# Optimization experiments

Hardware: AMD Instinct MI355X
Metric: run time of the kernel (lower is better)

## Reference

```python
import jax, jax.numpy as jnp
import numpy as np

B, T, C = 128, 256, 384
H, D = 6, 64

def setup_inputs() -> dict:
    key = jax.random.key(0)
    ks = jax.random.split(key, 6)
    s = 1.0 / np.sqrt(C)
    return {
        "x": jax.random.normal(ks[0], (B, T, C), dtype=jnp.float32),
        "Wq": jax.random.normal(ks[1], (H, C, D), dtype=jnp.float32) * s,
        "Wk": jax.random.normal(ks[2], (H, C, D), dtype=jnp.float32) * s,
        "Wv": jax.random.normal(ks[3], (H, C, D), dtype=jnp.float32) * s,
        "Wp": jax.random.normal(ks[4], (C, C), dtype=jnp.float32) * s,
        "bp": jnp.zeros((C,), dtype=jnp.float32),
    }

def reference(x, Wq, Wk, Wv, Wp, bp):
    # per-head projections (all heads at once): [B,T,C] x [H,C,D] -> [B,H,T,D]
    q = jnp.einsum("btc,hcd->bhtd", x, Wq)
    k = jnp.einsum("btc,hcd->bhtd", x, Wk)
    v = jnp.einsum("btc,hcd->bhtd", x, Wv)
    scale = 1.0 / jnp.sqrt(jnp.asarray(D, dtype=x.dtype))
    # scores [B,H,T,T], causal mask, softmax
    wei = jnp.einsum("bhqd,bhkd->bhqk", q, k) * scale
    causal = jnp.tril(jnp.ones((T, T), dtype=bool))
    wei = jnp.where(causal, wei, -jnp.inf)
    wei = jax.nn.softmax(wei, axis=-1)
    # dropout layers are identity in eval mode
    out = jnp.einsum("bhqk,bhkd->bhqd", wei, v)
    # concat heads: [B,T,H*D]
    out = out.transpose(0, 2, 1, 3).reshape(B, T, H * D)
    return out @ Wp + bp
```

## Files before the change

kernel.cpp:

```cpp
#include <hip/hip_runtime.h>
#include <stdint.h>


typedef __attribute__((ext_vector_type(8))) short bf16x8;
typedef __attribute__((ext_vector_type(4))) float f32x4;
typedef __attribute__((ext_vector_type(16))) float f32x16;

__device__ __forceinline__ unsigned short f2b(float f) {
    union { float f; unsigned int u; } v; v.f = f;
    unsigned int u = v.u + 0x7fffu + ((v.u >> 16) & 1u);
    return (unsigned short)(u >> 16);
}

__device__ __forceinline__ unsigned int pk2(float lo, float hi) {
    return (unsigned int)f2b(lo) | ((unsigned int)f2b(hi) << 16);
}

__device__ __forceinline__ void gload_lds16(const void* g, void* lds) {
    auto gp = reinterpret_cast<const __attribute__((address_space(1))) uint32_t*>(
        reinterpret_cast<uintptr_t>(g));
    auto lp = reinterpret_cast<__attribute__((address_space(3))) uint32_t*>(
        reinterpret_cast<uintptr_t>(lds));
    __builtin_amdgcn_global_load_lds(gp, lp, 16, 0, 0);
}

#define SBAR0() __builtin_amdgcn_sched_barrier(0)


__global__ void cvt_x_kernel(const float* __restrict__ x, unsigned short* __restrict__ xb, int n8) {
    int i = blockIdx.x * 256 + threadIdx.x;
    if (i >= n8) return;
    float4 a = ((const float4*)x)[(size_t)i * 2];
    float4 b = ((const float4*)x)[(size_t)i * 2 + 1];
    uint4 o;
    o.x = pk2(a.x, a.y); o.y = pk2(a.z, a.w);
    o.z = pk2(b.x, b.y); o.w = pk2(b.z, b.w);
    ((uint4*)xb)[i] = o;
}

__global__ void cvt_w_kernel(const float* __restrict__ Wq, const float* __restrict__ Wk,
                             const float* __restrict__ Wv, const float* __restrict__ Wp,
                             unsigned short* __restrict__ wt, unsigned short* __restrict__ wpt) {
    int i = blockIdx.x * 256 + threadIdx.x;
    if (i >= 589824) return;
    if (i < 442368) {
        int j = i / 384, c = i - j * 384;
        int p = j / 384, rem = j - p * 384;
        int h = rem >> 6, d = rem & 63;
        const float* W = (p == 0) ? Wq : ((p == 1) ? Wk : Wv);
        wt[i] = f2b(W[(size_t)(h * 384 + c) * 64 + d]);
    } else {
        int i2 = i - 442368;
        int n = i2 / 384, c = i2 - n * 384;
        wpt[i2] = f2b(Wp[(size_t)c * 384 + n]);
    }
}


__global__ __launch_bounds__(256, 3) void gemm_qkv(
    const unsigned short* __restrict__ xb,
    const unsigned short* __restrict__ wt,
    unsigned short* __restrict__ qO,
    unsigned short* __restrict__ kO,
    unsigned short* __restrict__ vO)
{
    extern __shared__ __align__(16) unsigned short smem[];
    unsigned short* AsBase = smem;
    unsigned short* BsBase = smem + 12288;

    const int tid  = threadIdx.x;
    const int lane = tid & 63;
    const int w    = tid >> 6;
    const int wm = w >> 1, wn = w & 1;

    const int flat = blockIdx.y * 9 + blockIdx.x;
    const int swz = (flat & 7) * 288 + (flat >> 3);
    const int bx = swz % 9, by = swz / 9;
    const int col0 = bx * 128;
    const int row0 = by * 128;

    const unsigned short* Abase = xb + (size_t)row0 * 384;
    const unsigned short* Bbase = wt + (size_t)col0 * 384;

    f32x4 acc[4][4];
#pragma unroll
    for (int mf = 0; mf < 4; ++mf)
#pragma unroll
        for (int nf = 0; nf < 4; ++nf)
#pragma unroll
            for (int r = 0; r < 4; ++r) acc[mf][nf][r] = 0.f;

    const int ci0 = tid;
    const int ci1 = tid + 256;
    const unsigned short* aSrc0 = Abase + (size_t)(ci0 >> 2) * 384 + (ci0 & 3) * 8;
    const unsigned short* aSrc1 = Abase + (size_t)(ci1 >> 2) * 384 + (ci1 & 3) * 8;
    const unsigned short* bSrc0 = Bbase + (size_t)(ci0 >> 2) * 384 + (ci0 & 3) * 8;
    const unsigned short* bSrc1 = Bbase + (size_t)(ci1 >> 2) * 384 + (ci1 & 3) * 8;
    const int cb = w * 64;

    auto STAGE = [&](int buf, int kt) {
        const int k0_ = kt * 32;
        gload_lds16(aSrc0 + k0_, AsBase + buf * 4096 + (cb + 0) * 8);
        gload_lds16(bSrc0 + k0_, BsBase + buf * 4096 + (cb + 0) * 8);
        gload_lds16(aSrc1 + k0_, AsBase + buf * 4096 + (cb + 256) * 8);
        gload_lds16(bSrc1 + k0_, BsBase + buf * 4096 + (cb + 256) * 8);
    };

    auto COMPUTE = [&](int buf) {
        const unsigned short* A = AsBase + buf * 4096;
        const unsigned short* B = BsBase + buf * 4096;
        bf16x8 aF[4], bF[4];
#pragma unroll
        for (int mf = 0; mf < 4; ++mf)
            aF[mf] = *(const bf16x8*)&A[(wm * 64 + mf * 16 + (lane & 15)) * 32 + (lane >> 4) * 8];
#pragma unroll
        for (int nf = 0; nf < 4; ++nf)
            bF[nf] = *(const bf16x8*)&B[(wn * 64 + nf * 16 + (lane & 15)) * 32 + (lane >> 4) * 8];
#pragma unroll
        for (int mf = 0; mf < 4; ++mf)
#pragma unroll
            for (int nf = 0; nf < 4; ++nf)
                acc[mf][nf] = __builtin_amdgcn_mfma_f32_16x16x32_bf16(aF[mf], bF[nf], acc[mf][nf], 0, 0, 0);
    };

    STAGE(0, 0);
    STAGE(1, 1);
    SBAR0();
    int bufS = 2, bufC = 0;
    for (int t = 0; t < 10; ++t) {
        STAGE(bufS, t + 2);
        bufS = (bufS == 2) ? 0 : bufS + 1;
        SBAR0();
        asm volatile("s_waitcnt vmcnt(8)" ::: "memory");
        SBAR0();
        __builtin_amdgcn_s_barrier();
        SBAR0();
        COMPUTE(bufC);
        bufC = (bufC == 2) ? 0 : bufC + 1;
        SBAR0();
        __builtin_amdgcn_s_barrier();
        SBAR0();
    }
    asm volatile("s_waitcnt vmcnt(4)" ::: "memory");
    SBAR0();
    __builtin_amdgcn_s_barrier();
    SBAR0();
    COMPUTE(1);
    SBAR0();
    __builtin_amdgcn_s_barrier();
    SBAR0();
    asm volatile("s_waitcnt vmcnt(0)" ::: "memory");
    SBAR0();
    __builtin_amdgcn_s_barrier();
    SBAR0();
    COMPUTE(2);
    __syncthreads();

    unsigned short* Ct = smem;
    const int co = tid & 15;
    const int rr = tid >> 4;
    const int colg = col0 + co * 8;
    const int p = colg / 384;
    const int rem = colg - p * 384;
    const int h = rem >> 6;
    const int d = rem & 63;
    unsigned short* dst = (p == 0) ? qO : ((p == 1) ? kO : vO);

#pragma unroll
    for (int ph = 0; ph < 2; ++ph) {
        if (wm == ph) {
#pragma unroll
            for (int mf = 0; mf < 4; ++mf)
#pragma unroll
                for (int nf = 0; nf < 4; ++nf)
#pragma unroll
                    for (int r = 0; r < 4; ++r)
                        Ct[(mf * 16 + (lane >> 4) * 4 + r) * 136 + wn * 64 + nf * 16 + (lane & 15)] =
                            f2b(acc[mf][nf][r]);
        }
        __syncthreads();
#pragma unroll
        for (int it = 0; it < 4; ++it) {
            const int r_loc = it * 16 + rr;
            const int m = row0 + ph * 64 + r_loc;
            const int b = m >> 8, t = m & 255;
            uint4 val = *(const uint4*)&Ct[r_loc * 136 + co * 8];
            *(uint4*)&dst[(size_t)((b * 6 + h) * 256 + t) * 64 + d] = val;
        }
        __syncthreads();
    }
}


__global__ __launch_bounds__(512) void attn_kernel(
    const unsigned short* __restrict__ Qg,
    const unsigned short* __restrict__ Kg,
    const unsigned short* __restrict__ Vg,
    unsigned short* __restrict__ Og)
{
    __shared__ __align__(16) unsigned short Ks[256 * 72];
    __shared__ __align__(16) unsigned short Vs[64 * 264];
    __shared__ __align__(16) unsigned short Ot[8 * 32 * 72];
    const int bh = blockIdx.x;
    const int b = bh / 6, h = bh - b * 6;
    const int tid = threadIdx.x;
    const int lane = tid & 63;
    const int w = tid >> 6;
    const int lo = lane & 31, hi = lane >> 5;

    const unsigned short* kg = Kg + (size_t)bh * 256 * 64;
#pragma unroll
    for (int j = 0; j < 4; ++j) {
        int chunk = tid + 512 * j;
        int key = chunk >> 3, dc = (chunk & 7) * 8;
        *(uint4*)&Ks[key * 72 + dc] = *(const uint4*)&kg[key * 64 + dc];
    }
    {
        const unsigned short* vg = Vg + (size_t)bh * 256 * 64;
        uint32_t* Vs32 = (uint32_t*)Vs;
#pragma unroll
        for (int i = 0; i < 2; ++i) {
            int u = tid + 512 * i;
            int t2 = (u & 31) | ((u >> 8) << 5);
            int dm = (u >> 5) & 7;
            uint4 r0 = *(const uint4*)&vg[(2 * t2 + 0) * 64 + dm * 8];
            uint4 r1 = *(const uint4*)&vg[(2 * t2 + 1) * 64 + dm * 8];
            const unsigned short* e0 = (const unsigned short*)&r0;
            const unsigned short* e1 = (const unsigned short*)&r1;
#pragma unroll
            for (int j = 0; j < 8; ++j)
                Vs32[(dm * 8 + j) * 132 + t2] = (uint32_t)e0[j] | ((uint32_t)e1[j] << 16);
        }
    }
    __syncthreads();

    const int q0 = w * 32;
    const unsigned short* qg = Qg + (size_t)bh * 256 * 64 + (size_t)(q0 + lo) * 64 + hi * 8;
    bf16x8 qF[4];
#pragma unroll
    for (int dc = 0; dc < 4; ++dc) qF[dc] = *(const bf16x8*)(qg + dc * 16);

    float m = -1e30f, ssum = 0.f;
    f32x16 o0, o1;
#pragma unroll
    for (int r = 0; r < 16; ++r) { o0[r] = 0.f; o1[r] = 0.f; }

    for (int kt = 0; kt <= w; ++kt) {
        f32x16 s;
#pragma unroll
        for (int r = 0; r < 16; ++r) s[r] = 0.f;
#pragma unroll
        for (int dc = 0; dc < 4; ++dc) {
            bf16x8 aK = *(const bf16x8*)&Ks[(kt * 32 + lo) * 72 + dc * 16 + hi * 8];
            s = __builtin_amdgcn_mfma_f32_32x32x16_bf16(aK, qF[dc], s, 0, 0, 0);
        }
        float p[16];
        float pmax = -1e30f;
        const bool diag = (kt == w);
#pragma unroll
        for (int r = 0; r < 16; ++r) {
            float sv = s[r] * 0.125f;
            const int keyl = (r & 3) + 8 * (r >> 2) + 4 * hi;
            if (diag && keyl > lo) sv = -1e30f;
            p[r] = sv;
            pmax = fmaxf(pmax, sv);
        }
        pmax = fmaxf(pmax, __shfl_xor(pmax, 32, 64));
        const float mn = fmaxf(m, pmax);
        const float sf = __expf(m - mn);
        m = mn;
        ssum *= sf;
#pragma unroll
        for (int r = 0; r < 16; ++r) { o0[r] *= sf; o1[r] *= sf; }
        float rs = 0.f;
#pragma unroll
        for (int r = 0; r < 16; ++r) { p[r] = __expf(p[r] - m); rs += p[r]; }
        rs += __shfl_xor(rs, 32, 64);
        ssum += rs;

        union { unsigned short u[16]; bf16x8 v[2]; } P;
        {
            float recv[4];
#pragma unroll
            for (int j2 = 0; j2 < 4; ++j2) {
                float sendv = hi ? p[j2] : p[4 + j2];
                recv[j2] = __shfl_xor(sendv, 32, 64);
            }
#pragma unroll
            for (int i = 0; i < 4; ++i) P.u[i]     = f2b(hi ? recv[i] : p[i]);
#pragma unroll
            for (int i = 0; i < 4; ++i) P.u[4 + i] = f2b(hi ? p[4 + i] : recv[i]);
        }
        {
            float recv[4];
#pragma unroll
            for (int j2 = 0; j2 < 4; ++j2) {
                float sendv = hi ? p[8 + j2] : p[12 + j2];
                recv[j2] = __shfl_xor(sendv, 32, 64);
            }
#pragma unroll
            for (int i = 0; i < 4; ++i) P.u[8 + i]  = f2b(hi ? recv[i] : p[8 + i]);
#pragma unroll
            for (int i = 0; i < 4; ++i) P.u[12 + i] = f2b(hi ? p[12 + i] : recv[i]);
        }

#pragma unroll
        for (int kc = 0; kc < 2; ++kc) {
            bf16x8 aV0 = *(const bf16x8*)&Vs[lo * 264 + kt * 32 + kc * 16 + hi * 8];
            o0 = __builtin_amdgcn_mfma_f32_32x32x16_bf16(aV0, P.v[kc], o0, 0, 0, 0);
            bf16x8 aV1 = *(const bf16x8*)&Vs[(32 + lo) * 264 + kt * 32 + kc * 16 + hi * 8];
            o1 = __builtin_amdgcn_mfma_f32_32x32x16_bf16(aV1, P.v[kc], o1, 0, 0, 0);
        }
    }

    const float inv = 1.f / ssum;
    {
        uint32_t* ot32 = (uint32_t*)&Ot[w * 32 * 72];
#pragma unroll
        for (int g = 0; g < 4; ++g) {
            const int dbase0 = 8 * g + 4 * hi;
            uint32_t w0 = pk2(o0[4 * g + 0] * inv, o0[4 * g + 1] * inv);
            uint32_t w1 = pk2(o0[4 * g + 2] * inv, o0[4 * g + 3] * inv);
            int dw = lo * 36 + (dbase0 >> 1);
            ot32[dw] = w0;
            ot32[dw + 1] = w1;
            uint32_t w2 = pk2(o1[4 * g + 0] * inv, o1[4 * g + 1] * inv);
            uint32_t w3 = pk2(o1[4 * g + 2] * inv, o1[4 * g + 3] * inv);
            int dw1 = lo * 36 + ((32 + dbase0) >> 1);
            ot32[dw1] = w2;
            ot32[dw1 + 1] = w3;
        }
    }
    __syncthreads();
    {
        const unsigned short* ot = &Ot[w * 32 * 72];
        const int q = lane >> 1;
        const int half = (lane & 1) * 32;
        unsigned short* og = Og + (size_t)(b * 256 + q0 + q) * 384 + h * 64 + half;
#pragma unroll
        for (int jj = 0; jj < 4; ++jj) {
            uint4 val = *(const uint4*)&ot[q * 72 + half + jj * 8];
            *(uint4*)&og[jj * 8] = val;
        }
    }
}


__global__ __launch_bounds__(256, 3) void gemm_proj(
    const unsigned short* __restrict__ ob,
    const unsigned short* __restrict__ wpt,
    const float* __restrict__ bp,
    float* __restrict__ out)
{
    __shared__ __align__(16) unsigned short As[3][128 * 32];
    __shared__ __align__(16) unsigned short Bs[3][128 * 32];
    const int tid  = threadIdx.x;
    const int lane = tid & 63;
    const int w    = tid >> 6;
    const int wm = w >> 1, wn = w & 1;

    const int flat = blockIdx.y * 3 + blockIdx.x;
    const int swz = (flat & 7) * 96 + (flat >> 3);
    const int bx = swz % 3, by = swz / 3;
    const int col0 = bx * 128;
    const int row0 = by * 128;

    const unsigned short* Abase = ob  + (size_t)row0 * 384;
    const unsigned short* Bbase = wpt + (size_t)col0 * 384;

    f32x4 acc[4][4];
#pragma unroll
    for (int mf = 0; mf < 4; ++mf)
#pragma unroll
        for (int nf = 0; nf < 4; ++nf)
#pragma unroll
            for (int r = 0; r < 4; ++r) acc[mf][nf][r] = 0.f;

    const int ci0 = tid;
    const int ci1 = tid + 256;
    const unsigned short* aSrc0 = Abase + (size_t)(ci0 >> 2) * 384 + (ci0 & 3) * 8;
    const unsigned short* aSrc1 = Abase + (size_t)(ci1 >> 2) * 384 + (ci1 & 3) * 8;
    const unsigned short* bSrc0 = Bbase + (size_t)(ci0 >> 2) * 384 + (ci0 & 3) * 8;
    const unsigned short* bSrc1 = Bbase + (size_t)(ci1 >> 2) * 384 + (ci1 & 3) * 8;
    const int cb = w * 64;

    auto STAGE = [&](int buf, int kt) {
        const int k0_ = kt * 32;
        gload_lds16(aSrc0 + k0_, (unsigned short*)As[buf] + (cb + 0) * 8);
        gload_lds16(bSrc0 + k0_, (unsigned short*)Bs[buf] + (cb + 0) * 8);
        gload_lds16(aSrc1 + k0_, (unsigned short*)As[buf] + (cb + 256) * 8);
        gload_lds16(bSrc1 + k0_, (unsigned short*)Bs[buf] + (cb + 256) * 8);
    };

    auto COMPUTE = [&](int buf) {
        const unsigned short* A = As[buf];
        const unsigned short* B = Bs[buf];
        bf16x8 aF[4], bF[4];
#pragma unroll
        for (int mf = 0; mf < 4; ++mf)
            aF[mf] = *(const bf16x8*)&A[(wm * 64 + mf * 16 + (lane & 15)) * 32 + (lane >> 4) * 8];
#pragma unroll
        for (int nf = 0; nf < 4; ++nf)
            bF[nf] = *(const bf16x8*)&B[(wn * 64 + nf * 16 + (lane & 15)) * 32 + (lane >> 4) * 8];
#pragma unroll
        for (int mf = 0; mf < 4; ++mf)
#pragma unroll
            for (int nf = 0; nf < 4; ++nf)
                acc[mf][nf] = __builtin_amdgcn_mfma_f32_16x16x32_bf16(aF[mf], bF[nf], acc[mf][nf], 0, 0, 0);
    };

    STAGE(0, 0);
    STAGE(1, 1);
    SBAR0();
    int bufS = 2, bufC = 0;
    for (int t = 0; t < 10; ++t) {
        STAGE(bufS, t + 2);
        bufS = (bufS == 2) ? 0 : bufS + 1;
        SBAR0();
        asm volatile("s_waitcnt vmcnt(8)" ::: "memory");
        SBAR0();
        __builtin_amdgcn_s_barrier();
        SBAR0();
        COMPUTE(bufC);
        bufC = (bufC == 2) ? 0 : bufC + 1;
        SBAR0();
        __builtin_amdgcn_s_barrier();
        SBAR0();
    }
    asm volatile("s_waitcnt vmcnt(4)" ::: "memory");
    SBAR0();
    __builtin_amdgcn_s_barrier();
    SBAR0();
    COMPUTE(1);
    SBAR0();
    __builtin_amdgcn_s_barrier();
    SBAR0();
    asm volatile("s_waitcnt vmcnt(0)" ::: "memory");
    SBAR0();
    __builtin_amdgcn_s_barrier();
    SBAR0();
    COMPUTE(2);

#pragma unroll
    for (int nf = 0; nf < 4; ++nf) {
        const int col = col0 + wn * 64 + nf * 16 + (lane & 15);
        const float bias = bp[col];
#pragma unroll
        for (int mf = 0; mf < 4; ++mf) {
            const int mbase = row0 + wm * 64 + mf * 16 + ((lane >> 4) * 4);
#pragma unroll
            for (int r = 0; r < 4; ++r) {
                const int mrow = mbase + r;
                out[(size_t)mrow * 384 + col] = acc[mf][nf][r] + bias;
            }
        }
    }
}


extern "C" void kernel_launch(void* const* d_in, const int* in_sizes, int n_in,
                              void* d_out, int out_size, void* d_ws, size_t ws_size,
                              hipStream_t stream) {
    const float* x  = (const float*)d_in[0];
    const float* Wq = (const float*)d_in[1];
    const float* Wk = (const float*)d_in[2];
    const float* Wv = (const float*)d_in[3];
    const float* Wp = (const float*)d_in[4];
    const float* bp = (const float*)d_in[5];
    float* out = (float*)d_out;

    char* ws = (char*)d_ws;
    unsigned short* xb  = (unsigned short*)(ws);
    unsigned short* qb  = (unsigned short*)(ws + 25165824);
    unsigned short* kb  = (unsigned short*)(ws + 50331648);
    unsigned short* vb  = (unsigned short*)(ws + 75497472);
    unsigned short* wt  = (unsigned short*)(ws + 100663296);
    unsigned short* wpt = (unsigned short*)(ws + 101548032);

    cvt_x_kernel<<<6144, 256, 0, stream>>>(x, xb, 1572864);
    cvt_w_kernel<<<2304, 256, 0, stream>>>(Wq, Wk, Wv, Wp, wt, wpt);
    gemm_qkv<<<dim3(9, 256), 256, 49152, stream>>>(xb, wt, qb, kb, vb);
    attn_kernel<<<768, 512, 0, stream>>>(qb, kb, vb, xb);
    gemm_proj<<<dim3(3, 256), 256, 0, stream>>>(xb, wpt, bp, out);
}
```

Baseline: 118.9 us.

## Fuse x fp32-to-bf16 conversion into QKV GEMM A-tile loading

Removes the separate x conversion kernel. gemm_qkv now loads fp32 x straight into registers, converts it to bf16 and writes it to double-buffered LDS, while B still arrives through async global-to-LDS loads. The pipeline drops from triple to double buffering, occupancy hint rises to 4, and the attention kernel's output staging now reuses the K/V LDS through dynamic shared memory. This saves one full write and reread of the bf16 x copy, at the cost of reading fp32 x (twice the bytes) once for each of the 9 column tiles, plus register-path conversion work inside the GEMM loop.

```diff
diff --git a/kernel.cpp b/kernel.cpp
--- a/kernel.cpp
+++ b/kernel.cpp
@@ -26,17 +26,6 @@
 
 #define SBAR0() __builtin_amdgcn_sched_barrier(0)
 
-
-__global__ void cvt_x_kernel(const float* __restrict__ x, unsigned short* __restrict__ xb, int n8) {
-    int i = blockIdx.x * 256 + threadIdx.x;
-    if (i >= n8) return;
-    float4 a = ((const float4*)x)[(size_t)i * 2];
-    float4 b = ((const float4*)x)[(size_t)i * 2 + 1];
-    uint4 o;
-    o.x = pk2(a.x, a.y); o.y = pk2(a.z, a.w);
-    o.z = pk2(b.x, b.y); o.w = pk2(b.z, b.w);
-    ((uint4*)xb)[i] = o;
-}
 
 __global__ void cvt_w_kernel(const float* __restrict__ Wq, const float* __restrict__ Wk,
                              const float* __restrict__ Wv, const float* __restrict__ Wp,
@@ -57,16 +46,18 @@
 }
 
 
-__global__ __launch_bounds__(256, 3) void gemm_qkv(
-    const unsigned short* __restrict__ xb,
+__global__ __launch_bounds__(256, 4) void gemm_qkv(
+    const float* __restrict__ x,
     const unsigned short* __restrict__ wt,
     unsigned short* __restrict__ qO,
     unsigned short* __restrict__ kO,
     unsigned short* __restrict__ vO)
 {
     extern __shared__ __align__(16) unsigned short smem[];
-    unsigned short* AsBase = smem;
-    unsigned short* BsBase = smem + 12288;
+    unsigned short* As0 = smem;
+    unsigned short* As1 = smem + 4096;
+    unsigned short* Bs0 = smem + 8192;
+    unsigned short* Bs1 = smem + 12288;
 
     const int tid  = threadIdx.x;
     const int lane = tid & 63;
@@ -79,8 +70,290 @@
     const int col0 = bx * 128;
     const int row0 = by * 128;
 
-    const unsigned short* Abase = xb + (size_t)row0 * 384;
-    const unsigned short* Bbase = wt + (size_t)col0 * 384;
+    f32x4 acc[4][4];
+#pragma unroll
+    for (int mf = 0; mf < 4; ++mf)
+#pragma unroll
+        for (int nf = 0; nf < 4; ++nf)
+#pragma unroll
+            for (int r = 0; r < 4; ++r) acc[mf][nf][r] = 0.f;
+
+    const int ci0 = tid;
+    const int ci1 = tid + 256;
+    const float* aS0 = x + (size_t)(row0 + (ci0 >> 2)) * 384 + (ci0 & 3) * 8;
+    const float* aS1 = x + (size_t)(row0 + (ci1 >> 2)) * 384 + (ci1 & 3) * 8;
+    const unsigned short* bS0 = wt + (size_t)(col0 + (ci0 >> 2)) * 384 + (ci0 & 3) * 8;
+    const unsigned short* bS1 = wt + (size_t)(col0 + (ci1 >> 2)) * 384 + (ci1 & 3) * 8;
+    const int cb = w * 64;
+
+    float4 aReg0, aReg1, aReg2, aReg3;
+    auto LOADA = [&](int kt) {
+        const float* p0 = aS0 + kt * 32;
+        const float* p1 = aS1 + kt * 32;
+        aReg0 = *(const float4*)(p0);
+        aReg1 = *(const float4*)(p0 + 4);
+        aReg2 = *(const float4*)(p1);
+        aReg3 = *(const float4*)(p1 + 4);
+    };
+    auto WRITEA = [&](unsigned short* As) {
+        uint4 w0 = make_uint4(pk2(aReg0.x, aReg0.y), pk2(aReg0.z, aReg0.w),
+                              pk2(aReg1.x, aReg1.y), pk2(aReg1.z, aReg1.w));
+        uint4 w1 = make_uint4(pk2(aReg2.x, aReg2.y), pk2(aReg2.z, aReg2.w),
+                              pk2(aReg3.x, aReg3.y), pk2(aReg3.z, aReg3.w));
+        *(uint4*)&As[ci0 * 8] = w0;
+        *(uint4*)&As[ci1 * 8] = w1;
+    };
+    auto STAGEB = [&](unsigned short* Bs, int kt) {
+        gload_lds16(bS0 + kt * 32, Bs + (cb + 0) * 8);
+        gload_lds16(bS1 + kt * 32, Bs + (cb + 256) * 8);
+    };
+    auto COMPUTE = [&](const unsigned short* A, const unsigned short* B) {
+        bf16x8 aF[4], bF[4];
+#pragma unroll
+        for (int mf = 0; mf < 4; ++mf)
+            aF[mf] = *(const bf16x8*)&A[(wm * 64 + mf * 16 + (lane & 15)) * 32 + (lane >> 4) * 8];
+#pragma unroll
+        for (int nf = 0; nf < 4; ++nf)
+            bF[nf] = *(const bf16x8*)&B[(wn * 64 + nf * 16 + (lane & 15)) * 32 + (lane >> 4) * 8];
+#pragma unroll
+        for (int mf = 0; mf < 4; ++mf)
+#pragma unroll
+            for (int nf = 0; nf < 4; ++nf)
+                acc[mf][nf] = __builtin_amdgcn_mfma_f32_16x16x32_bf16(aF[mf], bF[nf], acc[mf][nf], 0, 0, 0);
+    };
+
+    LOADA(0);
+    STAGEB(Bs0, 0);
+    WRITEA(As0);
+    __syncthreads();
+
+    for (int t = 0; t < 12; ++t) {
+        unsigned short* Acur = (t & 1) ? As1 : As0;
+        unsigned short* Bcur = (t & 1) ? Bs1 : Bs0;
+        unsigned short* Anx  = (t & 1) ? As0 : As1;
+        unsigned short* Bnx  = (t & 1) ? Bs0 : Bs1;
+        if (t < 11) {
+            LOADA(t + 1);
+            STAGEB(Bnx, t + 1);
+        }
+        COMPUTE(Acur, Bcur);
+        if (t < 11) WRITEA(Anx);
+        __syncthreads();
+    }
+
+    unsigned short* Ct = smem;
+    const int co = tid & 15;
+    const int rr = tid >> 4;
+    const int colg = col0 + co * 8;
+    const int p = colg / 384;
+    const int rem = colg - p * 384;
+    const int h = rem >> 6;
+    const int d = rem & 63;
+    unsigned short* dst = (p == 0) ? qO : ((p == 1) ? kO : vO);
+
+#pragma unroll
+    for (int ph = 0; ph < 2; ++ph) {
+        if (wm == ph) {
+#pragma unroll
+            for (int mf = 0; mf < 4; ++mf)
+#pragma unroll
+                for (int nf = 0; nf < 4; ++nf)
+#pragma unroll
+                    for (int r = 0; r < 4; ++r)
+                        Ct[(mf * 16 + (lane >> 4) * 4 + r) * 136 + wn * 64 + nf * 16 + (lane & 15)] =
+                            f2b(acc[mf][nf][r]);
+        }
+        __syncthreads();
+#pragma unroll
+        for (int it = 0; it < 4; ++it) {
+            const int r_loc = it * 16 + rr;
+            const int m = row0 + ph * 64 + r_loc;
+            const int b = m >> 8, t = m & 255;
+            uint4 val = *(const uint4*)&Ct[r_loc * 136 + co * 8];
+            *(uint4*)&dst[(size_t)((b * 6 + h) * 256 + t) * 64 + d] = val;
+        }
+        __syncthreads();
+    }
+}
+
+
+__global__ __launch_bounds__(512, 4) void attn_kernel(
+    const unsigned short* __restrict__ Qg,
+    const unsigned short* __restrict__ Kg,
+    const unsigned short* __restrict__ Vg,
+    unsigned short* __restrict__ Og)
+{
+    extern __shared__ __align__(16) unsigned short asmem[];
+    unsigned short* Ks = asmem;
+    unsigned short* Vs = asmem + 256 * 72;
+    unsigned short* Ot = asmem;
+    const int bh = blockIdx.x;
+    const int b = bh / 6, h = bh - b * 6;
+    const int tid = threadIdx.x;
+    const int lane = tid & 63;
+    const int w = tid >> 6;
+    const int lo = lane & 31, hi = lane >> 5;
+
+    const unsigned short* kg = Kg + (size_t)bh * 256 * 64;
+#pragma unroll
+    for (int j = 0; j < 4; ++j) {
+        int chunk = tid + 512 * j;
+        int key = chunk >> 3, dc = (chunk & 7) * 8;
+        *(uint4*)&Ks[key * 72 + dc] = *(const uint4*)&kg[key * 64 + dc];
+    }
+    {
+        const unsigned short* vg = Vg + (size_t)bh * 256 * 64;
+        uint32_t* Vs32 = (uint32_t*)Vs;
+#pragma unroll
+        for (int i = 0; i < 2; ++i) {
+            int u = tid + 512 * i;
+            int t2 = (u & 31) | ((u >> 8) << 5);
+            int dm = (u >> 5) & 7;
+            uint4 r0 = *(const uint4*)&vg[(2 * t2 + 0) * 64 + dm * 8];
+            uint4 r1 = *(const uint4*)&vg[(2 * t2 + 1) * 64 + dm * 8];
+            const unsigned short* e0 = (const unsigned short*)&r0;
+            const unsigned short* e1 = (const unsigned short*)&r1;
+#pragma unroll
+            for (int j = 0; j < 8; ++j)
+                Vs32[(dm * 8 + j) * 132 + t2] = (uint32_t)e0[j] | ((uint32_t)e1[j] << 16);
+        }
+    }
+    __syncthreads();
+
+    const int q0 = w * 32;
+    const unsigned short* qg = Qg + (size_t)bh * 256 * 64 + (size_t)(q0 + lo) * 64 + hi * 8;
+    bf16x8 qF[4];
+#pragma unroll
+    for (int dc = 0; dc < 4; ++dc) qF[dc] = *(const bf16x8*)(qg + dc * 16);
+
+    float m = -1e30f, ssum = 0.f;
+    f32x16 o0, o1;
+#pragma unroll
+    for (int r = 0; r < 16; ++r) { o0[r] = 0.f; o1[r] = 0.f; }
+
+    for (int kt = 0; kt <= w; ++kt) {
+        f32x16 s;
+#pragma unroll
+        for (int r = 0; r < 16; ++r) s[r] = 0.f;
+#pragma unroll
+        for (int dc = 0; dc < 4; ++dc) {
+            bf16x8 aK = *(const bf16x8*)&Ks[(kt * 32 + lo) * 72 + dc * 16 + hi * 8];
+            s = __builtin_amdgcn_mfma_f32_32x32x16_bf16(aK, qF[dc], s, 0, 0, 0);
+        }
+        float p[16];
+        float pmax = -1e30f;
+        const bool diag = (kt == w);
+#pragma unroll
+        for (int r = 0; r < 16; ++r) {
+            float sv = s[r] * 0.125f;
+            const int keyl = (r & 3) + 8 * (r >> 2) + 4 * hi;
+            if (diag && keyl > lo) sv = -1e30f;
+            p[r] = sv;
+            pmax = fmaxf(pmax, sv);
+        }
+        pmax = fmaxf(pmax, __shfl_xor(pmax, 32, 64));
+        const float mn = fmaxf(m, pmax);
+        const float sf = __expf(m - mn);
+        m = mn;
+        ssum *= sf;
+#pragma unroll
+        for (int r = 0; r < 16; ++r) { o0[r] *= sf; o1[r] *= sf; }
+        float rs = 0.f;
+#pragma unroll
+        for (int r = 0; r < 16; ++r) { p[r] = __expf(p[r] - m); rs += p[r]; }
+        rs += __shfl_xor(rs, 32, 64);
+        ssum += rs;
+
+        union { unsigned short u[16]; bf16x8 v[2]; } P;
+        {
+            float recv[4];
+#pragma unroll
+            for (int j2 = 0; j2 < 4; ++j2) {
+                float sendv = hi ? p[j2] : p[4 + j2];
+                recv[j2] = __shfl_xor(sendv, 32, 64);
+            }
+#pragma unroll
+            for (int i = 0; i < 4; ++i) P.u[i]     = f2b(hi ? recv[i] : p[i]);
+#pragma unroll
+            for (int i = 0; i < 4; ++i) P.u[4 + i] = f2b(hi ? p[4 + i] : recv[i]);
+        }
+        {
+            float recv[4];
+#pragma unroll
+            for (int j2 = 0; j2 < 4; ++j2) {
+                float sendv = hi ? p[8 + j2] : p[12 + j2];
+                recv[j2] = __shfl_xor(sendv, 32, 64);
+            }
+#pragma unroll
+            for (int i = 0; i < 4; ++i) P.u[8 + i]  = f2b(hi ? recv[i] : p[8 + i]);
+#pragma unroll
+            for (int i = 0; i < 4; ++i) P.u[12 + i] = f2b(hi ? p[12 + i] : recv[i]);
+        }
+
+#pragma unroll
+        for (int kc = 0; kc < 2; ++kc) {
+            bf16x8 aV0 = *(const bf16x8*)&Vs[lo * 264 + kt * 32 + kc * 16 + hi * 8];
+            o0 = __builtin_amdgcn_mfma_f32_32x32x16_bf16(aV0, P.v[kc], o0, 0, 0, 0);
+            bf16x8 aV1 = *(const bf16x8*)&Vs[(32 + lo) * 264 + kt * 32 + kc * 16 + hi * 8];
+            o1 = __builtin_amdgcn_mfma_f32_32x32x16_bf16(aV1, P.v[kc], o1, 0, 0, 0);
+        }
+    }
+
+    __syncthreads();
+    const float inv = 1.f / ssum;
+    {
+        uint32_t* ot32 = (uint32_t*)&Ot[w * 32 * 72];
+#pragma unroll
+        for (int g = 0; g < 4; ++g) {
+            const int dbase0 = 8 * g + 4 * hi;
+            uint32_t w0 = pk2(o0[4 * g + 0] * inv, o0[4 * g + 1] * inv);
+            uint32_t w1 = pk2(o0[4 * g + 2] * inv, o0[4 * g + 3] * inv);
+            int dw = lo * 36 + (dbase0 >> 1);
+            ot32[dw] = w0;
+            ot32[dw + 1] = w1;
+            uint32_t w2 = pk2(o1[4 * g + 0] * inv, o1[4 * g + 1] * inv);
+            uint32_t w3 = pk2(o1[4 * g + 2] * inv, o1[4 * g + 3] * inv);
+            int dw1 = lo * 36 + ((32 + dbase0) >> 1);
+            ot32[dw1] = w2;
+            ot32[dw1 + 1] = w3;
+        }
+    }
+    __syncthreads();
+    {
+        const unsigned short* ot = &Ot[w * 32 * 72];
+        const int q = lane >> 1;
+        const int half = (lane & 1) * 32;
+        unsigned short* og = Og + (size_t)(b * 256 + q0 + q) * 384 + h * 64 + half;
+#pragma unroll
+        for (int jj = 0; jj < 4; ++jj) {
+            uint4 val = *(const uint4*)&ot[q * 72 + half + jj * 8];
+            *(uint4*)&og[jj * 8] = val;
+        }
+    }
+}
+
+
+__global__ __launch_bounds__(256, 3) void gemm_proj(
+    const unsigned short* __restrict__ ob,
+    const unsigned short* __restrict__ wpt,
+    const float* __restrict__ bp,
+    float* __restrict__ out)
+{
+    __shared__ __align__(16) unsigned short As[3][128 * 32];
+    __shared__ __align__(16) unsigned short Bs[3][128 * 32];
+    const int tid  = threadIdx.x;
+    const int lane = tid & 63;
+    const int w    = tid >> 6;
+    const int wm = w >> 1, wn = w & 1;
+
+    const int flat = blockIdx.y * 3 + blockIdx.x;
+    const int swz = (flat & 7) * 96 + (flat >> 3);
+    const int bx = swz % 3, by = swz / 3;
+    const int col0 = bx * 128;
+    const int row0 = by * 128;
+
+    const unsigned short* Abase = ob  + (size_t)row0 * 384;
+    const unsigned short* Bbase = wpt + (size_t)col0 * 384;
 
     f32x4 acc[4][4];
 #pragma unroll
@@ -100,15 +373,15 @@
 
     auto STAGE = [&](int buf, int kt) {
         const int k0_ = kt * 32;
-        gload_lds16(aSrc0 + k0_, AsBase + buf * 4096 + (cb + 0) * 8);
-        gload_lds16(bSrc0 + k0_, BsBase + buf * 4096 + (cb + 0) * 8);
-        gload_lds16(aSrc1 + k0_, AsBase + buf * 4096 + (cb + 256) * 8);
-        gload_lds16(bSrc1 + k0_, BsBase + buf * 4096 + (cb + 256) * 8);
+        gload_lds16(aSrc0 + k0_, (unsigned short*)As[buf] + (cb + 0) * 8);
+        gload_lds16(bSrc0 + k0_, (unsigned short*)Bs[buf] + (cb + 0) * 8);
+        gload_lds16(aSrc1 + k0_, (unsigned short*)As[buf] + (cb + 256) * 8);
+        gload_lds16(bSrc1 + k0_, (unsigned short*)Bs[buf] + (cb + 256) * 8);
     };
 
     auto COMPUTE = [&](int buf) {
-        const unsigned short* A = AsBase + buf * 4096;
-        const unsigned short* B = BsBase + buf * 4096;
+        const unsigned short* A = As[buf];
+        const unsigned short* B = Bs[buf];
         bf16x8 aF[4], bF[4];
 #pragma unroll
         for (int mf = 0; mf < 4; ++mf)
@@ -154,292 +427,6 @@
     __builtin_amdgcn_s_barrier();
     SBAR0();
     COMPUTE(2);
-    __syncthreads();
-
-    unsigned short* Ct = smem;
-    const int co = tid & 15;
-    const int rr = tid >> 4;
-    const int colg = col0 + co * 8;
-    const int p = colg / 384;
-    const int rem = colg - p * 384;
-    const int h = rem >> 6;
-    const int d = rem & 63;
-    unsigned short* dst = (p == 0) ? qO : ((p == 1) ? kO : vO);
-
-#pragma unroll
-    for (int ph = 0; ph < 2; ++ph) {
-        if (wm == ph) {
-#pragma unroll
-            for (int mf = 0; mf < 4; ++mf)
-#pragma unroll
-                for (int nf = 0; nf < 4; ++nf)
-#pragma unroll
-                    for (int r = 0; r < 4; ++r)
-                        Ct[(mf * 16 + (lane >> 4) * 4 + r) * 136 + wn * 64 + nf * 16 + (lane & 15)] =
-                            f2b(acc[mf][nf][r]);
-        }
-        __syncthreads();
-#pragma unroll
-        for (int it = 0; it < 4; ++it) {
-            const int r_loc = it * 16 + rr;
-            const int m = row0 + ph * 64 + r_loc;
-            const int b = m >> 8, t = m & 255;
-            uint4 val = *(const uint4*)&Ct[r_loc * 136 + co * 8];
-            *(uint4*)&dst[(size_t)((b * 6 + h) * 256 + t) * 64 + d] = val;
-        }
-        __syncthreads();
-    }
-}
-
-
-__global__ __launch_bounds__(512) void attn_kernel(
-    const unsigned short* __restrict__ Qg,
-    const unsigned short* __restrict__ Kg,
-    const unsigned short* __restrict__ Vg,
-    unsigned short* __restrict__ Og)
-{
-    __shared__ __align__(16) unsigned short Ks[256 * 72];
-    __shared__ __align__(16) unsigned short Vs[64 * 264];
-    __shared__ __align__(16) unsigned short Ot[8 * 32 * 72];
-    const int bh = blockIdx.x;
-    const int b = bh / 6, h = bh - b * 6;
-    const int tid = threadIdx.x;
-    const int lane = tid & 63;
-    const int w = tid >> 6;
-    const int lo = lane & 31, hi = lane >> 5;
-
-    const unsigned short* kg = Kg + (size_t)bh * 256 * 64;
-#pragma unroll
-    for (int j = 0; j < 4; ++j) {
-        int chunk = tid + 512 * j;
-        int key = chunk >> 3, dc = (chunk & 7) * 8;
-        *(uint4*)&Ks[key * 72 + dc] = *(const uint4*)&kg[key * 64 + dc];
-    }
-    {
-        const unsigned short* vg = Vg + (size_t)bh * 256 * 64;
-        uint32_t* Vs32 = (uint32_t*)Vs;
-#pragma unroll
-        for (int i = 0; i < 2; ++i) {
-            int u = tid + 512 * i;
-            int t2 = (u & 31) | ((u >> 8) << 5);
-            int dm = (u >> 5) & 7;
-            uint4 r0 = *(const uint4*)&vg[(2 * t2 + 0) * 64 + dm * 8];
-            uint4 r1 = *(const uint4*)&vg[(2 * t2 + 1) * 64 + dm * 8];
-            const unsigned short* e0 = (const unsigned short*)&r0;
-            const unsigned short* e1 = (const unsigned short*)&r1;
-#pragma unroll
-            for (int j = 0; j < 8; ++j)
-                Vs32[(dm * 8 + j) * 132 + t2] = (uint32_t)e0[j] | ((uint32_t)e1[j] << 16);
-        }
-    }
-    __syncthreads();
-
-    const int q0 = w * 32;
-    const unsigned short* qg = Qg + (size_t)bh * 256 * 64 + (size_t)(q0 + lo) * 64 + hi * 8;
-    bf16x8 qF[4];
-#pragma unroll
-    for (int dc = 0; dc < 4; ++dc) qF[dc] = *(const bf16x8*)(qg + dc * 16);
-
-    float m = -1e30f, ssum = 0.f;
-    f32x16 o0, o1;
-#pragma unroll
-    for (int r = 0; r < 16; ++r) { o0[r] = 0.f; o1[r] = 0.f; }
-
-    for (int kt = 0; kt <= w; ++kt) {
-        f32x16 s;
-#pragma unroll
-        for (int r = 0; r < 16; ++r) s[r] = 0.f;
-#pragma unroll
-        for (int dc = 0; dc < 4; ++dc) {
-            bf16x8 aK = *(const bf16x8*)&Ks[(kt * 32 + lo) * 72 + dc * 16 + hi * 8];
-            s = __builtin_amdgcn_mfma_f32_32x32x16_bf16(aK, qF[dc], s, 0, 0, 0);
-        }
-        float p[16];
-        float pmax = -1e30f;
-        const bool diag = (kt == w);
-#pragma unroll
-        for (int r = 0; r < 16; ++r) {
-            float sv = s[r] * 0.125f;
-            const int keyl = (r & 3) + 8 * (r >> 2) + 4 * hi;
-            if (diag && keyl > lo) sv = -1e30f;
-            p[r] = sv;
-            pmax = fmaxf(pmax, sv);
-        }
-        pmax = fmaxf(pmax, __shfl_xor(pmax, 32, 64));
-        const float mn = fmaxf(m, pmax);
-        const float sf = __expf(m - mn);
-        m = mn;
-        ssum *= sf;
-#pragma unroll
-        for (int r = 0; r < 16; ++r) { o0[r] *= sf; o1[r] *= sf; }
-        float rs = 0.f;
-#pragma unroll
-        for (int r = 0; r < 16; ++r) { p[r] = __expf(p[r] - m); rs += p[r]; }
-        rs += __shfl_xor(rs, 32, 64);
-        ssum += rs;
-
-        union { unsigned short u[16]; bf16x8 v[2]; } P;
-        {
-            float recv[4];
-#pragma unroll
-            for (int j2 = 0; j2 < 4; ++j2) {
-                float sendv = hi ? p[j2] : p[4 + j2];
-                recv[j2] = __shfl_xor(sendv, 32, 64);
-            }
-#pragma unroll
-            for (int i = 0; i < 4; ++i) P.u[i]     = f2b(hi ? recv[i] : p[i]);
-#pragma unroll
-            for (int i = 0; i < 4; ++i) P.u[4 + i] = f2b(hi ? p[4 + i] : recv[i]);
-        }
-        {
-            float recv[4];
-#pragma unroll
-            for (int j2 = 0; j2 < 4; ++j2) {
-                float sendv = hi ? p[8 + j2] : p[12 + j2];
-                recv[j2] = __shfl_xor(sendv, 32, 64);
-            }
-#pragma unroll
-            for (int i = 0; i < 4; ++i) P.u[8 + i]  = f2b(hi ? recv[i] : p[8 + i]);
-#pragma unroll
-            for (int i = 0; i < 4; ++i) P.u[12 + i] = f2b(hi ? p[12 + i] : recv[i]);
-        }
-
-#pragma unroll
-        for (int kc = 0; kc < 2; ++kc) {
-            bf16x8 aV0 = *(const bf16x8*)&Vs[lo * 264 + kt * 32 + kc * 16 + hi * 8];
-            o0 = __builtin_amdgcn_mfma_f32_32x32x16_bf16(aV0, P.v[kc], o0, 0, 0, 0);
-            bf16x8 aV1 = *(const bf16x8*)&Vs[(32 + lo) * 264 + kt * 32 + kc * 16 + hi * 8];
-            o1 = __builtin_amdgcn_mfma_f32_32x32x16_bf16(aV1, P.v[kc], o1, 0, 0, 0);
-        }
-    }
-
-    const float inv = 1.f / ssum;
-    {
-        uint32_t* ot32 = (uint32_t*)&Ot[w * 32 * 72];
-#pragma unroll
-        for (int g = 0; g < 4; ++g) {
-            const int dbase0 = 8 * g + 4 * hi;
-            uint32_t w0 = pk2(o0[4 * g + 0] * inv, o0[4 * g + 1] * inv);
-            uint32_t w1 = pk2(o0[4 * g + 2] * inv, o0[4 * g + 3] * inv);
-            int dw = lo * 36 + (dbase0 >> 1);
-            ot32[dw] = w0;
-            ot32[dw + 1] = w1;
-            uint32_t w2 = pk2(o1[4 * g + 0] * inv, o1[4 * g + 1] * inv);
-            uint32_t w3 = pk2(o1[4 * g + 2] * inv, o1[4 * g + 3] * inv);
-            int dw1 = lo * 36 + ((32 + dbase0) >> 1);
-            ot32[dw1] = w2;
-            ot32[dw1 + 1] = w3;
-        }
-    }
-    __syncthreads();
-    {
-        const unsigned short* ot = &Ot[w * 32 * 72];
-        const int q = lane >> 1;
-        const int half = (lane & 1) * 32;
-        unsigned short* og = Og + (size_t)(b * 256 + q0 + q) * 384 + h * 64 + half;
-#pragma unroll
-        for (int jj = 0; jj < 4; ++jj) {
-            uint4 val = *(const uint4*)&ot[q * 72 + half + jj * 8];
-            *(uint4*)&og[jj * 8] = val;
-        }
-    }
-}
-
-
-__global__ __launch_bounds__(256, 3) void gemm_proj(
-    const unsigned short* __restrict__ ob,
-    const unsigned short* __restrict__ wpt,
-    const float* __restrict__ bp,
-    float* __restrict__ out)
-{
-    __shared__ __align__(16) unsigned short As[3][128 * 32];
-    __shared__ __align__(16) unsigned short Bs[3][128 * 32];
-    const int tid  = threadIdx.x;
-    const int lane = tid & 63;
-    const int w    = tid >> 6;
-    const int wm = w >> 1, wn = w & 1;
-
-    const int flat = blockIdx.y * 3 + blockIdx.x;
-    const int swz = (flat & 7) * 96 + (flat >> 3);
-    const int bx = swz % 3, by = swz / 3;
-    const int col0 = bx * 128;
-    const int row0 = by * 128;
-
-    const unsigned short* Abase = ob  + (size_t)row0 * 384;
-    const unsigned short* Bbase = wpt + (size_t)col0 * 384;
-
-    f32x4 acc[4][4];
-#pragma unroll
-    for (int mf = 0; mf < 4; ++mf)
-#pragma unroll
-        for (int nf = 0; nf < 4; ++nf)
-#pragma unroll
-            for (int r = 0; r < 4; ++r) acc[mf][nf][r] = 0.f;
-
-    const int ci0 = tid;
-    const int ci1 = tid + 256;
-    const unsigned short* aSrc0 = Abase + (size_t)(ci0 >> 2) * 384 + (ci0 & 3) * 8;
-    const unsigned short* aSrc1 = Abase + (size_t)(ci1 >> 2) * 384 + (ci1 & 3) * 8;
-    const unsigned short* bSrc0 = Bbase + (size_t)(ci0 >> 2) * 384 + (ci0 & 3) * 8;
-    const unsigned short* bSrc1 = Bbase + (size_t)(ci1 >> 2) * 384 + (ci1 & 3) * 8;
-    const int cb = w * 64;
-
-    auto STAGE = [&](int buf, int kt) {
-        const int k0_ = kt * 32;
-        gload_lds16(aSrc0 + k0_, (unsigned short*)As[buf] + (cb + 0) * 8);
-        gload_lds16(bSrc0 + k0_, (unsigned short*)Bs[buf] + (cb + 0) * 8);
-        gload_lds16(aSrc1 + k0_, (unsigned short*)As[buf] + (cb + 256) * 8);
-        gload_lds16(bSrc1 + k0_, (unsigned short*)Bs[buf] + (cb + 256) * 8);
-    };
-
-    auto COMPUTE = [&](int buf) {
-        const unsigned short* A = As[buf];
-        const unsigned short* B = Bs[buf];
-        bf16x8 aF[4], bF[4];
-#pragma unroll
-        for (int mf = 0; mf < 4; ++mf)
-            aF[mf] = *(const bf16x8*)&A[(wm * 64 + mf * 16 + (lane & 15)) * 32 + (lane >> 4) * 8];
-#pragma unroll
-        for (int nf = 0; nf < 4; ++nf)
-            bF[nf] = *(const bf16x8*)&B[(wn * 64 + nf * 16 + (lane & 15)) * 32 + (lane >> 4) * 8];
-#pragma unroll
-        for (int mf = 0; mf < 4; ++mf)
-#pragma unroll
-            for (int nf = 0; nf < 4; ++nf)
-                acc[mf][nf] = __builtin_amdgcn_mfma_f32_16x16x32_bf16(aF[mf], bF[nf], acc[mf][nf], 0, 0, 0);
-    };
-
-    STAGE(0, 0);
-    STAGE(1, 1);
-    SBAR0();
-    int bufS = 2, bufC = 0;
-    for (int t = 0; t < 10; ++t) {
-        STAGE(bufS, t + 2);
-        bufS = (bufS == 2) ? 0 : bufS + 1;
-        SBAR0();
-        asm volatile("s_waitcnt vmcnt(8)" ::: "memory");
-        SBAR0();
-        __builtin_amdgcn_s_barrier();
-        SBAR0();
-        COMPUTE(bufC);
-        bufC = (bufC == 2) ? 0 : bufC + 1;
-        SBAR0();
-        __builtin_amdgcn_s_barrier();
-        SBAR0();
-    }
-    asm volatile("s_waitcnt vmcnt(4)" ::: "memory");
-    SBAR0();
-    __builtin_amdgcn_s_barrier();
-    SBAR0();
-    COMPUTE(1);
-    SBAR0();
-    __builtin_amdgcn_s_barrier();
-    SBAR0();
-    asm volatile("s_waitcnt vmcnt(0)" ::: "memory");
-    SBAR0();
-    __builtin_amdgcn_s_barrier();
-    SBAR0();
-    COMPUTE(2);
 
 #pragma unroll
     for (int nf = 0; nf < 4; ++nf) {
@@ -470,16 +457,15 @@
     float* out = (float*)d_out;
 
     char* ws = (char*)d_ws;
-    unsigned short* xb  = (unsigned short*)(ws);
+    unsigned short* ob  = (unsigned short*)(ws);
     unsigned short* qb  = (unsigned short*)(ws + 25165824);
     unsigned short* kb  = (unsigned short*)(ws + 50331648);
     unsigned short* vb  = (unsigned short*)(ws + 75497472);
     unsigned short* wt  = (unsigned short*)(ws + 100663296);
     unsigned short* wpt = (unsigned short*)(ws + 101548032);
 
-    cvt_x_kernel<<<6144, 256, 0, stream>>>(x, xb, 1572864);
     cvt_w_kernel<<<2304, 256, 0, stream>>>(Wq, Wk, Wv, Wp, wt, wpt);
-    gemm_qkv<<<dim3(9, 256), 256, 49152, stream>>>(xb, wt, qb, kb, vb);
-    attn_kernel<<<768, 512, 0, stream>>>(qb, kb, vb, xb);
-    gemm_proj<<<dim3(3, 256), 256, 0, stream>>>(xb, wpt, bp, out);
-}
+    gemm_qkv<<<dim3(9, 256), 256, 32768, stream>>>(x, wt, qb, kb, vb);
+    attn_kernel<<<768, 512, 70656, stream>>>(qb, kb, vb, ob);
+    gemm_proj<<<dim3(3, 256), 256, 0, stream>>>(ob, wpt, bp, out);
+}
```

Result: faster. 107.8 us (-9.3%).

## Swizzle GEMM LDS tiles and alias attention output buffer to cut LDS

Applied to the files above, without the earlier changes.

Both GEMM kernels now apply an XOR swizzle to the 16-byte chunk column when staging A/B tiles into LDS, with matching reads in the fragment loads. This is meant to avoid LDS bank conflicts on the MFMA operand reads. The attention kernel moves to dynamic shared memory, reuses the K buffer region for the output staging tile (with an added barrier), and requests 4 waves per SIMD via launch bounds. Together these aim at lower LDS footprint and higher occupancy, at the cost of an extra sync and possible register pressure from the occupancy hint.

```diff
diff --git a/kernel.cpp b/kernel.cpp
--- a/kernel.cpp
+++ b/kernel.cpp
@@ -92,10 +92,12 @@
 
     const int ci0 = tid;
     const int ci1 = tid + 256;
-    const unsigned short* aSrc0 = Abase + (size_t)(ci0 >> 2) * 384 + (ci0 & 3) * 8;
-    const unsigned short* aSrc1 = Abase + (size_t)(ci1 >> 2) * 384 + (ci1 & 3) * 8;
-    const unsigned short* bSrc0 = Bbase + (size_t)(ci0 >> 2) * 384 + (ci0 & 3) * 8;
-    const unsigned short* bSrc1 = Bbase + (size_t)(ci1 >> 2) * 384 + (ci1 & 3) * 8;
+    const int r0c = ci0 >> 2, o0c = (ci0 & 3) ^ ((ci0 >> 3) & 3);
+    const int r1c = ci1 >> 2, o1c = (ci1 & 3) ^ ((ci1 >> 3) & 3);
+    const unsigned short* aSrc0 = Abase + (size_t)r0c * 384 + o0c * 8;
+    const unsigned short* aSrc1 = Abase + (size_t)r1c * 384 + o1c * 8;
+    const unsigned short* bSrc0 = Bbase + (size_t)r0c * 384 + o0c * 8;
+    const unsigned short* bSrc1 = Bbase + (size_t)r1c * 384 + o1c * 8;
     const int cb = w * 64;
 
     auto STAGE = [&](int buf, int kt) {
@@ -106,16 +108,19 @@
         gload_lds16(bSrc1 + k0_, BsBase + buf * 4096 + (cb + 256) * 8);
     };
 
+    const int fr = lane & 15;
+    const int oc = (lane >> 4) ^ ((fr >> 1) & 3);
+
     auto COMPUTE = [&](int buf) {
         const unsigned short* A = AsBase + buf * 4096;
         const unsigned short* B = BsBase + buf * 4096;
         bf16x8 aF[4], bF[4];
 #pragma unroll
         for (int mf = 0; mf < 4; ++mf)
-            aF[mf] = *(const bf16x8*)&A[(wm * 64 + mf * 16 + (lane & 15)) * 32 + (lane >> 4) * 8];
+            aF[mf] = *(const bf16x8*)&A[(wm * 64 + mf * 16 + fr) * 32 + oc * 8];
 #pragma unroll
         for (int nf = 0; nf < 4; ++nf)
-            bF[nf] = *(const bf16x8*)&B[(wn * 64 + nf * 16 + (lane & 15)) * 32 + (lane >> 4) * 8];
+            bF[nf] = *(const bf16x8*)&B[(wn * 64 + nf * 16 + fr) * 32 + oc * 8];
 #pragma unroll
         for (int mf = 0; mf < 4; ++mf)
 #pragma unroll
@@ -192,15 +197,16 @@
 }
 
 
-__global__ __launch_bounds__(512) void attn_kernel(
+__global__ __launch_bounds__(512, 4) void attn_kernel(
     const unsigned short* __restrict__ Qg,
     const unsigned short* __restrict__ Kg,
     const unsigned short* __restrict__ Vg,
     unsigned short* __restrict__ Og)
 {
-    __shared__ __align__(16) unsigned short Ks[256 * 72];
-    __shared__ __align__(16) unsigned short Vs[64 * 264];
-    __shared__ __align__(16) unsigned short Ot[8 * 32 * 72];
+    extern __shared__ __align__(16) unsigned short asmem[];
+    unsigned short* Ks = asmem;
+    unsigned short* Vs = asmem + 256 * 72;
+    unsigned short* Ot = asmem;
     const int bh = blockIdx.x;
     const int b = bh / 6, h = bh - b * 6;
     const int tid = threadIdx.x;
@@ -313,6 +319,7 @@
         }
     }
 
+    __syncthreads();
     const float inv = 1.f / ssum;
     {
         uint32_t* ot32 = (uint32_t*)&Ot[w * 32 * 72];
@@ -378,10 +385,12 @@
 
     const int ci0 = tid;
     const int ci1 = tid + 256;
-    const unsigned short* aSrc0 = Abase + (size_t)(ci0 >> 2) * 384 + (ci0 & 3) * 8;
-    const unsigned short* aSrc1 = Abase + (size_t)(ci1 >> 2) * 384 + (ci1 & 3) * 8;
-    const unsigned short* bSrc0 = Bbase + (size_t)(ci0 >> 2) * 384 + (ci0 & 3) * 8;
-    const unsigned short* bSrc1 = Bbase + (size_t)(ci1 >> 2) * 384 + (ci1 & 3) * 8;
+    const int r0c = ci0 >> 2, o0c = (ci0 & 3) ^ ((ci0 >> 3) & 3);
+    const int r1c = ci1 >> 2, o1c = (ci1 & 3) ^ ((ci1 >> 3) & 3);
+    const unsigned short* aSrc0 = Abase + (size_t)r0c * 384 + o0c * 8;
+    const unsigned short* aSrc1 = Abase + (size_t)r1c * 384 + o1c * 8;
+    const unsigned short* bSrc0 = Bbase + (size_t)r0c * 384 + o0c * 8;
+    const unsigned short* bSrc1 = Bbase + (size_t)r1c * 384 + o1c * 8;
     const int cb = w * 64;
 
     auto STAGE = [&](int buf, int kt) {
@@ -392,16 +401,19 @@
         gload_lds16(bSrc1 + k0_, (unsigned short*)Bs[buf] + (cb + 256) * 8);
     };
 
+    const int fr = lane & 15;
+    const int oc = (lane >> 4) ^ ((fr >> 1) & 3);
+
     auto COMPUTE = [&](int buf) {
         const unsigned short* A = As[buf];
         const unsigned short* B = Bs[buf];
         bf16x8 aF[4], bF[4];
 #pragma unroll
         for (int mf = 0; mf < 4; ++mf)
-            aF[mf] = *(const bf16x8*)&A[(wm * 64 + mf * 16 + (lane & 15)) * 32 + (lane >> 4) * 8];
+            aF[mf] = *(const bf16x8*)&A[(wm * 64 + mf * 16 + fr) * 32 + oc * 8];
 #pragma unroll
         for (int nf = 0; nf < 4; ++nf)
-            bF[nf] = *(const bf16x8*)&B[(wn * 64 + nf * 16 + (lane & 15)) * 32 + (lane >> 4) * 8];
+            bF[nf] = *(const bf16x8*)&B[(wn * 64 + nf * 16 + fr) * 32 + oc * 8];
 #pragma unroll
         for (int mf = 0; mf < 4; ++mf)
 #pragma unroll
@@ -480,6 +492,6 @@
     cvt_x_kernel<<<6144, 256, 0, stream>>>(x, xb, 1572864);
     cvt_w_kernel<<<2304, 256, 0, stream>>>(Wq, Wk, Wv, Wp, wt, wpt);
     gemm_qkv<<<dim3(9, 256), 256, 49152, stream>>>(xb, wt, qb, kb, vb);
-    attn_kernel<<<768, 512, 0, stream>>>(qb, kb, vb, xb);
+    attn_kernel<<<768, 512, 70656, stream>>>(qb, kb, vb, xb);
     gemm_proj<<<dim3(3, 256), 256, 0, stream>>>(xb, wpt, bp, out);
 }
```

After: 109.8 us. 1.08x faster.
